# Performance work log

Hardware: AMD Instinct MI355X
Metric: run time of the kernel (lower is better)

The kernel has to match this reference:

```python
import jax, jax.numpy as jnp
import numpy as np

NUM_OBJ = 512   # batch_size(8) * objects_per_scene(64)
K = 16          # parts per object
N = NUM_OBJ * K # total part nodes = 8192
P = 512         # points per part
E = NUM_OBJ * K * (K - 1)  # 122880 directed intra-object edges


def setup_inputs() -> dict:
    key = jax.random.key(0)
    ks = jax.random.split(key, 16)

    def w(k, shape, fan_in):
        return jax.random.normal(k, shape, jnp.float32) / np.sqrt(fan_in)

    inp = {}
    inp["pcls_arr"] = jax.random.normal(ks[0], (N, P, 6), jnp.float32)
    # PointNetfeat pointwise convs (6->64->128->256), BN affine params
    inp["W1"] = w(ks[1], (6, 64), 6);     inp["b1"] = jnp.zeros(64);  inp["g1"] = jnp.ones(64);  inp["bt1"] = jnp.zeros(64)
    inp["W2"] = w(ks[2], (64, 128), 64);  inp["b2"] = jnp.zeros(128); inp["g2"] = jnp.ones(128); inp["bt2"] = jnp.zeros(128)
    inp["W3"] = w(ks[3], (128, 256), 128); inp["b3"] = jnp.zeros(256); inp["g3"] = jnp.ones(256); inp["bt3"] = jnp.zeros(256)
    # object_embedding Linear(256->256)
    inp["We"] = w(ks[4], (256, 256), 256); inp["be"] = jnp.zeros(256)
    # two GCN layers (256->256->256)
    inp["Wg1"] = w(ks[5], (256, 256), 256); inp["bg1"] = jnp.zeros(256)
    inp["Wg2"] = w(ks[6], (256, 256), 256); inp["bg2"] = jnp.zeros(256)
    # connectivity head: Linear(512->256), Linear(256->256), Linear(256->1)
    inp["Wc1"] = w(ks[7], (512, 256), 512); inp["bc1"] = jnp.zeros(256)
    inp["Wc2"] = w(ks[8], (256, 256), 256); inp["bc2"] = jnp.zeros(256)
    inp["Wc3"] = w(ks[9], (256, 1), 256);   inp["bc3"] = jnp.zeros(1)
    # dense intra-object directed edges (i != j), matching the nested-loop construction
    ii, jj = np.meshgrid(np.arange(K), np.arange(K), indexing="ij")
    m = ii != jj
    i_loc, j_loc = ii[m], jj[m]            # [K*(K-1)] local pair indices, row-major order
    base = (np.arange(NUM_OBJ) * K)[:, None]
    inp["edge_src"] = jnp.asarray((base + i_loc[None, :]).reshape(-1), jnp.int32)
    inp["edge_dst"] = jnp.asarray((base + j_loc[None, :]).reshape(-1), jnp.int32)
    inp["edge_obj"] = jnp.asarray(np.repeat(np.arange(NUM_OBJ), K * (K - 1)), jnp.int32)
    inp["edge_i"]   = jnp.asarray(np.tile(i_loc, NUM_OBJ), jnp.int32)
    inp["edge_j"]   = jnp.asarray(np.tile(j_loc, NUM_OBJ), jnp.int32)
    return inp


def _bn(x, g, bt):
    # eval-mode BatchNorm with running_mean=0, running_var=1 -> per-channel affine
    return x * g + bt


def _gcn_layer(x, W, b, edge_src, edge_dst):
    # GCNConv with self-loops and symmetric deg^{-1/2} normalization
    xw = x @ W                                               # [N, C]
    deg = jax.ops.segment_sum(jnp.ones(E, x.dtype), edge_dst, num_segments=N) + 1.0
    dinv = deg ** -0.5
    norm = dinv[edge_src] * dinv[edge_dst]                   # [E]
    agg = jax.ops.segment_sum(xw[edge_src] * norm[:, None], edge_dst, num_segments=N)
    agg = agg + xw * (1.0 / deg)[:, None]                    # self-loop term
    return agg + b


def reference(pcls_arr, W1, b1, g1, bt1, W2, b2, g2, bt2, W3, b3, g3, bt3,
              We, be, Wg1, bg1, Wg2, bg2, Wc1, bc1, Wc2, bc2, Wc3, bc3,
              edge_src, edge_dst, edge_obj, edge_i, edge_j):
    # PointNetfeat: pointwise MLP over points, max-pool -> [N, 256]
    h = jax.nn.relu(_bn(pcls_arr @ W1 + b1, g1, bt1))        # [N, P, 64]
    h = jax.nn.relu(_bn(h @ W2 + b2, g2, bt2))               # [N, P, 128]
    h = _bn(h @ W3 + b3, g3, bt3)                            # [N, P, 256]
    feat = jnp.max(h, axis=1)                                # [N, 256]
    emb = feat @ We + be                                     # object_embedding

    # MultiGCN: gcn -> relu -> gcn
    x = jax.nn.relu(_gcn_layer(emb, Wg1, bg1, edge_src, edge_dst))
    x = _gcn_layer(x, Wg2, bg2, edge_src, edge_dst)          # [N, 256]

    # gather parent/child embeddings, concat, connectivity MLP, tanh
    pair = jnp.concatenate([x[edge_src], x[edge_dst]], axis=1)  # [E, 512]
    c = jax.nn.relu(pair @ Wc1 + bc1)
    c = jax.nn.relu(c @ Wc2 + bc2)
    c = jnp.tanh((c @ Wc3 + bc3)[:, 0])                      # [E]

    # scatter edge scores into per-object KxK matrices (zero diagonal)
    out = jnp.zeros((NUM_OBJ, K, K), c.dtype).at[edge_obj, edge_i, edge_j].set(c)
    return out
```

## Files before the change

kernel.cpp:

```cpp
#include <hip/hip_runtime.h>
#include <hip/hip_bf16.h>
#include <stdint.h>
#include <stddef.h>


typedef short bf16x8 __attribute__((ext_vector_type(8)));
typedef short bf16x4 __attribute__((ext_vector_type(4)));
typedef float f32x4  __attribute__((ext_vector_type(4)));

#define WT1_OFF   0u
#define WT2_OFF   4096u
#define WT3_OFF   20480u
#define B1F_OFF   86016u
#define B2F_OFF   86272u
#define B3F_OFF   86784u

__device__ __forceinline__ unsigned short f2bf(float f) {
  union { float f; unsigned u; } v; v.f = f;
  unsigned r = v.u + 0x7fffu + ((v.u >> 16) & 1u);
  return (unsigned short)(r >> 16);
}

__device__ __forceinline__ bf16x4 pack_relu4(f32x4 d) {
  __hip_bfloat162 lo = __float22bfloat162_rn(make_float2(fmaxf(d.x, 0.f), fmaxf(d.y, 0.f)));
  __hip_bfloat162 hi = __float22bfloat162_rn(make_float2(fmaxf(d.z, 0.f), fmaxf(d.w, 0.f)));
  union { bf16x4 v; __hip_bfloat162 h[2]; } u;
  u.h[0] = lo; u.h[1] = hi;
  return u.v;
}

__global__ void prep_kernel(
    const float* __restrict__ W1, const float* __restrict__ b1,
    const float* __restrict__ g1, const float* __restrict__ bt1,
    const float* __restrict__ W2, const float* __restrict__ b2,
    const float* __restrict__ g2, const float* __restrict__ bt2,
    const float* __restrict__ W3, const float* __restrict__ b3,
    const float* __restrict__ g3, const float* __restrict__ bt3,
    unsigned char* __restrict__ ws)
{
  unsigned short* wt1 = (unsigned short*)(ws + WT1_OFF);
  unsigned short* wt2 = (unsigned short*)(ws + WT2_OFF);
  unsigned short* wt3 = (unsigned short*)(ws + WT3_OFF);
  float* b1f  = (float*)(ws + B1F_OFF);
  float* b2f  = (float*)(ws + B2F_OFF);
  float* b3f  = (float*)(ws + B3F_OFF);

  int i = blockIdx.x * 256 + threadIdx.x;
  if (i < 2048) { int o = i >> 5, c = i & 31;
    float v = (c < 6) ? W1[c*64 + o] * g1[o]
            : (c == 6 ? (b1[o]*g1[o] + bt1[o]) : 0.f);
    wt1[i] = f2bf(v); return; }
  i -= 2048;
  if (i < 8192) { int o = i >> 6, c = i & 63;
    wt2[i] = f2bf(W2[c*128 + o] * g2[o]); return; }
  i -= 8192;
  if (i < 32768) { int o = i >> 7, c = i & 127;
    wt3[i] = f2bf(W3[c*256 + o] * g3[o]); return; }
  i -= 32768;
  if (i < 64)  { b1f[i] = b1[i]*g1[i] + bt1[i]; return; }
  i -= 64;
  if (i < 128) { b2f[i] = b2[i]*g2[i] + bt2[i]; return; }
  i -= 128;
  if (i < 256) { b3f[i] = b3[i]*g3[i] + bt3[i]; }
}

#define LDSX  0
#define LDSH1 5120
#define LDSH2 14336

__global__ __launch_bounds__(512)
__attribute__((amdgpu_waves_per_eu(4, 4)))
void pointnet_fused_kernel(
    const float* __restrict__ pcls, const unsigned char* __restrict__ ws,
    const float* __restrict__ We,  const float* __restrict__ be,
    const float* __restrict__ Wg1, const float* __restrict__ bg1,
    const float* __restrict__ Wg2, const float* __restrict__ bg2,
    const float* __restrict__ Wc1, const float* __restrict__ bc1,
    const float* __restrict__ Wc2, const float* __restrict__ bc2,
    const float* __restrict__ Wc3, const float* __restrict__ bc3,
    float* __restrict__ out)
{
  __shared__ __align__(16) unsigned short lds[31744];

  const unsigned short* wt1 = (const unsigned short*)(ws + WT1_OFF);
  const unsigned short* wt2 = (const unsigned short*)(ws + WT2_OFF);
  const unsigned short* wt3 = (const unsigned short*)(ws + WT3_OFF);
  const float* b2f = (const float*)(ws + B2F_OFF);
  const float* b3f = (const float*)(ws + B3F_OFF);

  const int tid  = threadIdx.x;
  const int w    = tid >> 6;
  const int lane = tid & 63;
  const int l15  = lane & 15;
  const int q    = lane >> 4;
  const int obj  = blockIdx.x;

  const int c1t = w & 3;
  const int ph  = w >> 2;

  bf16x8 af1 = *(const bf16x8*)(wt1 + (c1t*16 + l15)*32 + q*8);
  bf16x8 af2[2], af3[2][4];
#pragma unroll
  for (int kf = 0; kf < 2; ++kf)
    af2[kf] = *(const bf16x8*)(wt2 + (w*16 + l15)*64 + kf*32 + q*8);
#pragma unroll
  for (int nt = 0; nt < 2; ++nt)
#pragma unroll
    for (int kf = 0; kf < 4; ++kf)
      af3[nt][kf] = *(const bf16x8*)(wt3 + ((2*w + nt)*16 + l15)*128 + kf*32 + q*8);

  const f32x4 bias2 = *(const f32x4*)(b2f + w*16 + q*4);

  const int i1v = tid < 256;
  int p0 = tid / 6,          c0 = tid - 6*p0;
  int p1 = (512 + tid) / 6,  c1 = (512 + tid) - 6*p1;
  const int soff0 = LDSX + p0*40 + c0;
  const int soff1 = LDSX + p1*40 + c1;

  for (int i = tid; i < 5120; i += 512) lds[i] = 0;
  __syncthreads();
  if (tid < 128) lds[LDSX + tid*40 + 6] = 0x3F80;

  const float* pbase = pcls + (size_t)obj * 49152;
  lds[soff0] = f2bf(pbase[tid]);
  if (i1v) lds[soff1] = f2bf(pbase[512 + tid]);
  __syncthreads();

  f32x4 macc[2];
  float sacc[2][4];
#pragma unroll
  for (int nt = 0; nt < 2; ++nt) {
    macc[nt] = (f32x4){-3e38f, -3e38f, -3e38f, -3e38f};
#pragma unroll
    for (int r = 0; r < 4; ++r) sacc[nt][r] = 0.f;
  }

#pragma unroll
  for (int i = 0; i < 4; ++i) {
    const int pt = ph*4 + i;
    bf16x8 b = *(const bf16x8*)(&lds[LDSX + (pt*16 + l15)*40 + q*8]);
    f32x4 d = {0.f, 0.f, 0.f, 0.f};
    d = __builtin_amdgcn_mfma_f32_16x16x32_bf16(af1, b, d, 0, 0, 0);
    *(bf16x4*)(&lds[LDSH1 + (pt*16 + l15)*72 + c1t*16 + q*4]) = pack_relu4(d);
  }
  __syncthreads();

  for (int cg = 0; cg < 64; ++cg) {
    const int havenext = (cg < 63);

    float pf0, pf1;
    if (havenext) {
      pf0 = pbase[(cg + 1)*768 + tid];
      if (i1v) pf1 = pbase[(cg + 1)*768 + 512 + tid];
    }
#pragma unroll
    for (int pt = 0; pt < 8; ++pt) {
      bf16x8 b0  = *(const bf16x8*)(&lds[LDSH1 + (pt*16 + l15)*72 + q*8]);
      bf16x8 b1v = *(const bf16x8*)(&lds[LDSH1 + (pt*16 + l15)*72 + 32 + q*8]);
      f32x4 d = bias2;
      d = __builtin_amdgcn_mfma_f32_16x16x32_bf16(af2[0], b0,  d, 0, 0, 0);
      d = __builtin_amdgcn_mfma_f32_16x16x32_bf16(af2[1], b1v, d, 0, 0, 0);
      *(bf16x4*)(&lds[LDSH2 + (pt*16 + l15)*136 + w*16 + q*4]) = pack_relu4(d);
    }
    if (havenext) {
      lds[soff0] = f2bf(pf0);
      if (i1v) lds[soff1] = f2bf(pf1);
    }
    __syncthreads();

    if (havenext) {
#pragma unroll
      for (int i = 0; i < 4; ++i) {
        const int pt = ph*4 + i;
        bf16x8 b = *(const bf16x8*)(&lds[LDSX + (pt*16 + l15)*40 + q*8]);
        f32x4 d = {0.f, 0.f, 0.f, 0.f};
        d = __builtin_amdgcn_mfma_f32_16x16x32_bf16(af1, b, d, 0, 0, 0);
        *(bf16x4*)(&lds[LDSH1 + (pt*16 + l15)*72 + c1t*16 + q*4]) = pack_relu4(d);
      }
    }
#pragma unroll
    for (int pt = 0; pt < 8; ++pt) {
      bf16x8 b[4];
#pragma unroll
      for (int kf = 0; kf < 4; ++kf)
        b[kf] = *(const bf16x8*)(&lds[LDSH2 + (pt*16 + l15)*136 + kf*32 + q*8]);
#pragma unroll
      for (int nt = 0; nt < 2; ++nt) {
        f32x4 d = {0.f, 0.f, 0.f, 0.f};
#pragma unroll
        for (int kf = 0; kf < 4; ++kf)
          d = __builtin_amdgcn_mfma_f32_16x16x32_bf16(af3[nt][kf], b[kf], d, 0, 0, 0);
#pragma unroll
        for (int r = 0; r < 4; ++r)
          macc[nt][r] = fmaxf(macc[nt][r], d[r]);
      }
    }
    if ((cg & 3) == 3) {
#pragma unroll
      for (int nt = 0; nt < 2; ++nt) {
#pragma unroll
        for (int r = 0; r < 4; ++r) {
          float v = macc[nt][r];
          v = fmaxf(v, __shfl_xor(v, 1));
          v = fmaxf(v, __shfl_xor(v, 2));
          v = fmaxf(v, __shfl_xor(v, 4));
          v = fmaxf(v, __shfl_xor(v, 8));
          sacc[nt][r] += v;
        }
        macc[nt] = (f32x4){-3e38f, -3e38f, -3e38f, -3e38f};
      }
    }
    __syncthreads();
  }

  float* fls  = (float*)&lds[0];
  float* fs   = fls;
  float* bA   = fls + 256;
  float* bB   = fls + 512;
  float* part = fls + 768;
  float* redv = fls + 1280;

#pragma unroll
  for (int r = 0; r < 4; ++r) {
    if (l15 == r) {
#pragma unroll
      for (int nt = 0; nt < 2; ++nt) {
        const int ch = (2*w + nt)*16 + q*4 + r;
        fs[ch] = sacc[nt][r] + 16.f * b3f[ch];
      }
    }
  }
  __syncthreads();

  const int tt = tid & 255, hh = tid >> 8;
  const int cb = hh * 128;
  float a;

  a = 0.f;
#pragma unroll 8
  for (int c = 0; c < 128; ++c) a += fs[cb + c] * We[(cb + c)*256 + tt];
  part[hh*256 + tt] = a;
  __syncthreads();
  if (hh == 0) bA[tt] = part[tt] + part[256 + tt] + 16.f * be[tt];
  __syncthreads();

  a = 0.f;
#pragma unroll 8
  for (int c = 0; c < 128; ++c) a += bA[cb + c] * Wg1[(cb + c)*256 + tt];
  part[hh*256 + tt] = a;
  __syncthreads();
  if (hh == 0) bB[tt] = fmaxf((part[tt] + part[256 + tt]) * 0.0625f + bg1[tt], 0.f);
  __syncthreads();

  a = 0.f;
#pragma unroll 8
  for (int c = 0; c < 128; ++c) a += bB[cb + c] * Wg2[(cb + c)*256 + tt];
  part[hh*256 + tt] = a;
  __syncthreads();
  if (hh == 0) bA[tt] = part[tt] + part[256 + tt] + bg2[tt];
  __syncthreads();

  a = 0.f;
#pragma unroll 8
  for (int c = 0; c < 128; ++c) {
    const float xv = bA[cb + c];
    a += xv * Wc1[(cb + c)*256 + tt];
    a += xv * Wc1[(cb + c + 256)*256 + tt];
  }
  part[hh*256 + tt] = a;
  __syncthreads();
  if (hh == 0) bB[tt] = fmaxf(part[tt] + part[256 + tt] + bc1[tt], 0.f);
  __syncthreads();

  a = 0.f;
#pragma unroll 8
  for (int c = 0; c < 128; ++c) a += bB[cb + c] * Wc2[(cb + c)*256 + tt];
  part[hh*256 + tt] = a;
  __syncthreads();
  if (hh == 0) bA[tt] = fmaxf(part[tt] + part[256 + tt] + bc2[tt], 0.f);
  __syncthreads();

  float prod = (hh == 0) ? bA[tt] * Wc3[tt] : 0.f;
#pragma unroll
  for (int off = 1; off < 64; off <<= 1) prod += __shfl_xor(prod, off);
  if (lane == 0) redv[w] = prod;
  __syncthreads();
  if (tid == 0) redv[0] = tanhf(redv[0] + redv[1] + redv[2] + redv[3] + bc3[0]);
  __syncthreads();
  const float cv = redv[0];
  if (hh == 0)
    out[obj*256 + tt] = ((tt >> 4) == (tt & 15)) ? 0.f : cv;
}

extern "C" void kernel_launch(void* const* d_in, const int* in_sizes, int n_in,
                              void* d_out, int out_size, void* d_ws, size_t ws_size,
                              hipStream_t stream) {
  const float* pcls = (const float*)d_in[0];
  const float* W1 = (const float*)d_in[1];  const float* b1 = (const float*)d_in[2];
  const float* g1 = (const float*)d_in[3];  const float* bt1 = (const float*)d_in[4];
  const float* W2 = (const float*)d_in[5];  const float* b2 = (const float*)d_in[6];
  const float* g2 = (const float*)d_in[7];  const float* bt2 = (const float*)d_in[8];
  const float* W3 = (const float*)d_in[9];  const float* b3 = (const float*)d_in[10];
  const float* g3 = (const float*)d_in[11]; const float* bt3 = (const float*)d_in[12];
  const float* We = (const float*)d_in[13]; const float* be = (const float*)d_in[14];
  const float* Wg1 = (const float*)d_in[15]; const float* bg1 = (const float*)d_in[16];
  const float* Wg2 = (const float*)d_in[17]; const float* bg2 = (const float*)d_in[18];
  const float* Wc1 = (const float*)d_in[19]; const float* bc1 = (const float*)d_in[20];
  const float* Wc2 = (const float*)d_in[21]; const float* bc2 = (const float*)d_in[22];
  const float* Wc3 = (const float*)d_in[23]; const float* bc3 = (const float*)d_in[24];
  unsigned char* ws = (unsigned char*)d_ws;
  float* out = (float*)d_out;

  prep_kernel<<<170, 256, 0, stream>>>(W1, b1, g1, bt1, W2, b2, g2, bt2,
                                       W3, b3, g3, bt3, ws);
  pointnet_fused_kernel<<<512, 512, 0, stream>>>(
      pcls, ws, We, be, Wg1, bg1, Wg2, bg2, Wc1, bc1, Wc2, bc2, Wc3, bc3, out);
}
```

Baseline: 503.7 us.

## Retile layer-2 MFMA work per wave, vectorize point loads, keep max-sum in LDS

```diff
diff --git a/kernel.cpp b/kernel.cpp
--- a/kernel.cpp
+++ b/kernel.cpp
@@ -67,6 +67,7 @@
 #define LDSX  0
 #define LDSH1 5120
 #define LDSH2 14336
+#define LDSFS 31744
 
 __global__ __launch_bounds__(512)
 __attribute__((amdgpu_waves_per_eu(4, 4)))
@@ -80,7 +81,7 @@
     const float* __restrict__ Wc3, const float* __restrict__ bc3,
     float* __restrict__ out)
 {
-  __shared__ __align__(16) unsigned short lds[31744];
+  __shared__ __align__(16) unsigned short lds[32256];
 
   const unsigned short* wt1 = (const unsigned short*)(ws + WT1_OFF);
   const unsigned short* wt2 = (const unsigned short*)(ws + WT2_OFF);
@@ -98,42 +99,48 @@
   const int c1t = w & 3;
   const int ph  = w >> 2;
 
+  const int ct2 = (w & 3) * 2;
+  const int pb2 = (w >> 2) * 4;
+
   bf16x8 af1 = *(const bf16x8*)(wt1 + (c1t*16 + l15)*32 + q*8);
-  bf16x8 af2[2], af3[2][4];
-#pragma unroll
-  for (int kf = 0; kf < 2; ++kf)
-    af2[kf] = *(const bf16x8*)(wt2 + (w*16 + l15)*64 + kf*32 + q*8);
+  bf16x8 af2[2][2], af3[2][4];
+#pragma unroll
+  for (int ct = 0; ct < 2; ++ct)
+#pragma unroll
+    for (int kf = 0; kf < 2; ++kf)
+      af2[ct][kf] = *(const bf16x8*)(wt2 + ((ct2 + ct)*16 + l15)*64 + kf*32 + q*8);
 #pragma unroll
   for (int nt = 0; nt < 2; ++nt)
 #pragma unroll
     for (int kf = 0; kf < 4; ++kf)
       af3[nt][kf] = *(const bf16x8*)(wt3 + ((2*w + nt)*16 + l15)*128 + kf*32 + q*8);
 
-  const f32x4 bias2 = *(const f32x4*)(b2f + w*16 + q*4);
-
-  const int i1v = tid < 256;
-  int p0 = tid / 6,          c0 = tid - 6*p0;
-  int p1 = (512 + tid) / 6,  c1 = (512 + tid) - 6*p1;
-  const int soff0 = LDSX + p0*40 + c0;
-  const int soff1 = LDSX + p1*40 + c1;
+  f32x4 bs2[2];
+#pragma unroll
+  for (int ct = 0; ct < 2; ++ct)
+    bs2[ct] = *(const f32x4*)(b2f + (ct2 + ct)*16 + q*4);
+
+  const int sv = tid < 384;
+  const int sp = tid / 3;
+  const int sc = tid % 3;
+  unsigned* ldsu = (unsigned*)lds;
 
   for (int i = tid; i < 5120; i += 512) lds[i] = 0;
+  if (tid < 256) ((float*)&lds[LDSFS])[tid] = 0.f;
   __syncthreads();
   if (tid < 128) lds[LDSX + tid*40 + 6] = 0x3F80;
 
   const float* pbase = pcls + (size_t)obj * 49152;
-  lds[soff0] = f2bf(pbase[tid]);
-  if (i1v) lds[soff1] = f2bf(pbase[512 + tid]);
+  if (sv) {
+    const float2 pv = *(const float2*)(pbase + 2*tid);
+    ldsu[sp*20 + sc] = (unsigned)f2bf(pv.x) | ((unsigned)f2bf(pv.y) << 16);
+  }
   __syncthreads();
 
   f32x4 macc[2];
-  float sacc[2][4];
-#pragma unroll
-  for (int nt = 0; nt < 2; ++nt) {
+#pragma unroll
+  for (int nt = 0; nt < 2; ++nt)
     macc[nt] = (f32x4){-3e38f, -3e38f, -3e38f, -3e38f};
-#pragma unroll
-    for (int r = 0; r < 4; ++r) sacc[nt][r] = 0.f;
-  }
 
 #pragma unroll
   for (int i = 0; i < 4; ++i) {
@@ -148,24 +155,24 @@
   for (int cg = 0; cg < 64; ++cg) {
     const int havenext = (cg < 63);
 
-    float pf0, pf1;
-    if (havenext) {
-      pf0 = pbase[(cg + 1)*768 + tid];
-      if (i1v) pf1 = pbase[(cg + 1)*768 + 512 + tid];
+    float2 pv;
+    if (havenext && sv)
+      pv = *(const float2*)(pbase + (cg + 1)*768 + 2*tid);
+#pragma unroll
+    for (int pt = 0; pt < 4; ++pt) {
+      const int ptt = pb2 + pt;
+      bf16x8 b0  = *(const bf16x8*)(&lds[LDSH1 + (ptt*16 + l15)*72 + q*8]);
+      bf16x8 b1v = *(const bf16x8*)(&lds[LDSH1 + (ptt*16 + l15)*72 + 32 + q*8]);
+#pragma unroll
+      for (int ct = 0; ct < 2; ++ct) {
+        f32x4 d = bs2[ct];
+        d = __builtin_amdgcn_mfma_f32_16x16x32_bf16(af2[ct][0], b0,  d, 0, 0, 0);
+        d = __builtin_amdgcn_mfma_f32_16x16x32_bf16(af2[ct][1], b1v, d, 0, 0, 0);
+        *(bf16x4*)(&lds[LDSH2 + (ptt*16 + l15)*136 + (ct2 + ct)*16 + q*4]) = pack_relu4(d);
+      }
     }
-#pragma unroll
-    for (int pt = 0; pt < 8; ++pt) {
-      bf16x8 b0  = *(const bf16x8*)(&lds[LDSH1 + (pt*16 + l15)*72 + q*8]);
-      bf16x8 b1v = *(const bf16x8*)(&lds[LDSH1 + (pt*16 + l15)*72 + 32 + q*8]);
-      f32x4 d = bias2;
-      d = __builtin_amdgcn_mfma_f32_16x16x32_bf16(af2[0], b0,  d, 0, 0, 0);
-      d = __builtin_amdgcn_mfma_f32_16x16x32_bf16(af2[1], b1v, d, 0, 0, 0);
-      *(bf16x4*)(&lds[LDSH2 + (pt*16 + l15)*136 + w*16 + q*4]) = pack_relu4(d);
-    }
-    if (havenext) {
-      lds[soff0] = f2bf(pf0);
-      if (i1v) lds[soff1] = f2bf(pf1);
-    }
+    if (havenext && sv)
+      ldsu[sp*20 + sc] = (unsigned)f2bf(pv.x) | ((unsigned)f2bf(pv.y) << 16);
     __syncthreads();
 
     if (havenext) {
@@ -196,6 +203,7 @@
       }
     }
     if ((cg & 3) == 3) {
+      float* fsacc = (float*)&lds[LDSFS];
 #pragma unroll
       for (int nt = 0; nt < 2; ++nt) {
 #pragma unroll
@@ -205,7 +213,7 @@
           v = fmaxf(v, __shfl_xor(v, 2));
           v = fmaxf(v, __shfl_xor(v, 4));
           v = fmaxf(v, __shfl_xor(v, 8));
-          sacc[nt][r] += v;
+          if (l15 == 0) fsacc[(2*w + nt)*16 + q*4 + r] += v;
         }
         macc[nt] = (f32x4){-3e38f, -3e38f, -3e38f, -3e38f};
       }
@@ -214,22 +222,13 @@
   }
 
   float* fls  = (float*)&lds[0];
-  float* fs   = fls;
-  float* bA   = fls + 256;
-  float* bB   = fls + 512;
-  float* part = fls + 768;
-  float* redv = fls + 1280;
-
-#pragma unroll
-  for (int r = 0; r < 4; ++r) {
-    if (l15 == r) {
-#pragma unroll
-      for (int nt = 0; nt < 2; ++nt) {
-        const int ch = (2*w + nt)*16 + q*4 + r;
-        fs[ch] = sacc[nt][r] + 16.f * b3f[ch];
-      }
-    }
-  }
+  float* fs   = (float*)&lds[LDSFS];
+  float* bA   = fls;
+  float* bB   = fls + 256;
+  float* part = fls + 512;
+  float* redv = fls + 1024;
+
+  if (tid < 256) fs[tid] += 16.f * b3f[tid];
   __syncthreads();
 
   const int tt = tid & 255, hh = tid >> 8;
```

Result: faster. 482.4 us (-4.2%).
